# Kernel tuning notes

Hardware: AMD Instinct MI355X
Metric: run time of the kernel (lower is better)

## Reference

```python
import jax, jax.numpy as jnp
import numpy as np

N, E, D, L = 100000, 1600000, 32, 5


def setup_inputs() -> dict:
    key = jax.random.key(0)
    ks = jax.random.split(key, 8)
    s = 1.0 / np.sqrt(D)
    return {
        "x": jax.random.normal(ks[0], (N, D), dtype=jnp.float32),
        "edge_attr": jax.random.normal(ks[1], (E, D), dtype=jnp.float32),
        "edge_index": jax.random.randint(ks[2], (2, E), 0, N, dtype=jnp.int64),
        "W1": jax.random.normal(ks[3], (L, D, D), dtype=jnp.float32) * s,
        "b1": jnp.zeros((L, D), dtype=jnp.float32),
        "W2": jax.random.normal(ks[4], (L, D, D), dtype=jnp.float32) * s,
        "b2": jnp.zeros((L, D), dtype=jnp.float32),
        "eps": jnp.zeros((L,), dtype=jnp.float32),  # train_eps=True, init 0
    }


def reference(x, edge_attr, edge_index, W1, b1, W2, b2, eps):
    # GINEConv x num_layers: aggr_i = sum_j relu(x_j + e_ij); out = MLP((1+eps)*x_i + aggr_i)
    src = edge_index[0]  # j (message source)
    dst = edge_index[1]  # i (message target)
    n = x.shape[0]
    for l in range(W1.shape[0]):
        msg = jax.nn.relu(x[src] + edge_attr)                  # [E, D]
        aggr = jax.ops.segment_sum(msg, dst, num_segments=n)    # [N, D]
        h = (1.0 + eps[l]) * x + aggr
        h = jax.nn.relu(h @ W1[l] + b1[l]) @ W2[l] + b2[l]      # inner MLP
        x = jax.nn.relu(h)                                      # outer relu in forward
    return x
```

## Files before the change

kernel.cpp:

```cpp
#include <hip/hip_runtime.h>

#define D 32
#define NPB 64
#define SRC_BITS 25
#define SRC_MASK ((1 << SRC_BITS) - 1)
#define SCAN_CHUNK 1024
#define PKCAP 2048

typedef unsigned short ushort_t;

__device__ __forceinline__ float relu_f(float v) { return v > 0.f ? v : 0.f; }

__device__ __forceinline__ unsigned bf16_rne(float f) {
    unsigned u = __float_as_uint(f);
    return (u + 0x7FFFu + ((u >> 16) & 1u)) >> 16;
}
__device__ __forceinline__ float bflo(unsigned u) { return __uint_as_float(u << 16); }
__device__ __forceinline__ float bfhi(unsigned u) { return __uint_as_float(u & 0xFFFF0000u); }

__global__ void __launch_bounds__(256) hist_kernel(
    const int* __restrict__ dst, int* __restrict__ deg, int E)
{
    int e = blockIdx.x * 256 + threadIdx.x;
    if (e < E) atomicAdd(&deg[dst[e]], 1);
}

__global__ void __launch_bounds__(256) scan_partial_kernel(
    const int* __restrict__ deg, int* __restrict__ part, int N)
{
    __shared__ int s[256];
    int t = threadIdx.x;
    int base = blockIdx.x * SCAN_CHUNK + t * 4;
    int sum = 0;
    #pragma unroll
    for (int i = 0; i < 4; ++i) { int idx = base + i; if (idx < N) sum += deg[idx]; }
    s[t] = sum;
    __syncthreads();
    for (int off = 128; off > 0; off >>= 1) {
        if (t < off) s[t] += s[t + off];
        __syncthreads();
    }
    if (t == 0) part[blockIdx.x] = s[0];
}

__global__ void scan_part_exclusive_kernel(int* part, int nb)
{
    if (threadIdx.x == 0 && blockIdx.x == 0) {
        int run = 0;
        for (int i = 0; i < nb; ++i) { int v = part[i]; part[i] = run; run += v; }
    }
}

__global__ void __launch_bounds__(256) scan_final_kernel(
    int* __restrict__ rowdeg, const int* __restrict__ part, int N)
{
    __shared__ int s[256];
    int t = threadIdx.x;
    int base = blockIdx.x * SCAN_CHUNK + t * 4;
    int d0 = 0, d1 = 0, d2 = 0, d3 = 0;
    if (base + 0 < N) d0 = rowdeg[base + 0];
    if (base + 1 < N) d1 = rowdeg[base + 1];
    if (base + 2 < N) d2 = rowdeg[base + 2];
    if (base + 3 < N) d3 = rowdeg[base + 3];
    int tsum = d0 + d1 + d2 + d3;
    s[t] = tsum;
    __syncthreads();
    for (int off = 1; off < 256; off <<= 1) {
        int a = (t >= off) ? s[t - off] : 0;
        __syncthreads();
        s[t] += a;
        __syncthreads();
    }
    int excl = s[t] - tsum + part[blockIdx.x];
    if (base + 0 < N) rowdeg[base + 0] = excl;
    if (base + 1 < N) rowdeg[base + 1] = excl + d0;
    if (base + 2 < N) rowdeg[base + 2] = excl + d0 + d1;
    if (base + 3 < N) rowdeg[base + 3] = excl + d0 + d1 + d2;
}

__global__ void __launch_bounds__(256) place_full_kernel(
    const int* __restrict__ src, const int* __restrict__ dst,
    const float* __restrict__ ea, int* __restrict__ row,
    int* __restrict__ srcpk, unsigned* __restrict__ eah, int E)
{
    int i = blockIdx.x * 256 + threadIdx.x;
    if (i >= E * 8) return;
    int e = i >> 3, q = i & 7;
    int pos = 0;
    if (q == 0) {
        int d = dst[e];
        pos = atomicAdd(&row[d], 1);
        srcpk[pos] = src[e] | ((d & (NPB - 1)) << SRC_BITS);
    }
    pos = __shfl(pos, 0, 8);
    float4 v = reinterpret_cast<const float4*>(ea)[(size_t)e * 8 + q];
    uint2 w;
    w.x = bf16_rne(v.x) | (bf16_rne(v.y) << 16);
    w.y = bf16_rne(v.z) | (bf16_rne(v.w) << 16);
    reinterpret_cast<uint2*>(eah)[(size_t)pos * 8 + q] = w;
}

__global__ void __launch_bounds__(256) place_csr_kernel(
    const int* __restrict__ src, const int* __restrict__ dst,
    int* __restrict__ row, int* __restrict__ srcperm,
    int* __restrict__ eperm, int E)
{
    int e = blockIdx.x * 256 + threadIdx.x;
    if (e < E) {
        int pos = atomicAdd(&row[dst[e]], 1);
        srcperm[pos] = src[e] | ((dst[e] & (NPB - 1)) << SRC_BITS);
        eperm[pos] = e;
    }
}

__global__ void __launch_bounds__(256) x2h_kernel(
    const float* __restrict__ x, ushort_t* __restrict__ xh, int n)
{
    int i = blockIdx.x * 256 + threadIdx.x;
    if (i < n) xh[i] = (ushort_t)bf16_rne(x[i]);
}

template <bool LAST>
__global__ void __launch_bounds__(256, 4) gine_fused7_kernel(
    const uint2* __restrict__ xh2,
    const uint2* __restrict__ eah,
    const int* __restrict__ srcpk, const int* __restrict__ row,
    const float* __restrict__ W1, const float* __restrict__ b1,
    const float* __restrict__ W2, const float* __restrict__ b2,
    const float* __restrict__ eps, int l,
    ushort_t* __restrict__ outh, float* __restrict__ outf, int N)
{
    __shared__ float aggr[NPB][D];
    __shared__ float W1s[D * D], W2s[D * D];
    __shared__ float b1s[D], b2s[D];
    __shared__ float ys[8][D];
    __shared__ int   pkL[PKCAP];

    int t = threadIdx.x;
    int n0 = blockIdx.x * NPB;
    int nlast = min(n0 + NPB - 1, N - 1);
    int estart = n0 ? row[n0 - 1] : 0;
    int eend   = row[nlast];
    int EB = eend - estart;
    int staged = min(EB, PKCAP);

    for (int i = t; i < D * D; i += 256) { W1s[i] = W1[i]; W2s[i] = W2[i]; }
    if (t < D) { b1s[t] = b1[t]; b2s[t] = b2[t]; }
    for (int i = t; i < NPB * D; i += 256) ((float*)aggr)[i] = 0.f;
    for (int i = t; i < staged; i += 256) pkL[i] = srcpk[estart + i];
    __syncthreads();

    int g8 = t >> 3;
    int q  = t & 7;

    int chunk = (staged + 31) >> 5;
    int a = min(g8 * chunk, staged);
    int b = min(a + chunk, staged);

    float4 acc = make_float4(0.f, 0.f, 0.f, 0.f);
    int cur = -1;

    auto flush = [&]() {
        if (cur >= 0) {
            atomicAdd(&aggr[cur][q * 4 + 0], acc.x);
            atomicAdd(&aggr[cur][q * 4 + 1], acc.y);
            atomicAdd(&aggr[cur][q * 4 + 2], acc.z);
            atomicAdd(&aggr[cur][q * 4 + 3], acc.w);
        }
    };
    auto edge = [&](int ld, uint2 ew, uint2 xw) {
        if (ld != cur) {
            flush();
            cur = ld;
            acc = make_float4(0.f, 0.f, 0.f, 0.f);
        }
        acc.x += relu_f(bflo(xw.x) + bflo(ew.x));
        acc.y += relu_f(bfhi(xw.x) + bfhi(ew.x));
        acc.z += relu_f(bflo(xw.y) + bflo(ew.y));
        acc.w += relu_f(bfhi(xw.y) + bfhi(ew.y));
    };

    uint2 wA[4], wB[4], xA[4], xB[4];
    int   pA[4], pB[4];

    auto loadA = [&](int base) {
        #pragma unroll
        for (int i = 0; i < 4; ++i) {
            int p = pkL[base + i];
            pA[i] = p;
            wA[i] = eah[(size_t)(estart + base + i) * 8 + q];
            xA[i] = xh2[(size_t)(p & SRC_MASK) * 8 + q];
        }
    };
    auto loadB = [&](int base) {
        #pragma unroll
        for (int i = 0; i < 4; ++i) {
            int p = pkL[base + i];
            pB[i] = p;
            wB[i] = eah[(size_t)(estart + base + i) * 8 + q];
            xB[i] = xh2[(size_t)(p & SRC_MASK) * 8 + q];
        }
    };
    auto computeA = [&]() {
        #pragma unroll
        for (int i = 0; i < 4; ++i)
            edge((pA[i] >> SRC_BITS) & (NPB - 1), wA[i], xA[i]);
    };
    auto computeB = [&]() {
        #pragma unroll
        for (int i = 0; i < 4; ++i)
            edge((pB[i] >> SRC_BITS) & (NPB - 1), wB[i], xB[i]);
    };

    int nfull = (b - a) >> 2;
    int k = a;
    if (nfull > 0) loadA(k);
    int i = 0;
    for (; i + 2 <= nfull; i += 2) {
        loadB(k + 4);
        computeA();
        if (i + 2 < nfull) loadA(k + 8);
        computeB();
        k += 8;
    }
    if (i < nfull) { computeA(); k += 4; }

    for (int e = k; e < b; ++e) {
        int p = pkL[e];
        uint2 w = eah[(size_t)(estart + e) * 8 + q];
        uint2 xw = xh2[(size_t)(p & SRC_MASK) * 8 + q];
        edge((p >> SRC_BITS) & (NPB - 1), w, xw);
    }
    if (EB > staged) {
        int ovn = EB - staged;
        int c2 = (ovn + 31) >> 5;
        int o0 = staged + min(g8 * c2, ovn);
        int o1 = min(o0 + c2, EB);
        for (int e = o0; e < o1; ++e) {
            int p = srcpk[estart + e];
            uint2 w = eah[(size_t)(estart + e) * 8 + q];
            uint2 xw = xh2[(size_t)(p & SRC_MASK) * 8 + q];
            edge((p >> SRC_BITS) & (NPB - 1), w, xw);
        }
    }
    flush();
    __syncthreads();

    const ushort_t* xhu = (const ushort_t*)xh2;
    int hw = t >> 5, j = t & 31;
    float ep1 = 1.0f + eps[l];
    for (int r = 0; r < 8; ++r) {
        int ln = hw * 8 + r;
        int n = n0 + ln;
        if (n >= N) break;
        float xf = bflo((unsigned)xhu[(size_t)n * D + j]);
        float h = ep1 * xf + aggr[ln][j];
        aggr[ln][j] = h;
        float a1 = b1s[j];
        #pragma unroll
        for (int kk = 0; kk < D; ++kk)
            a1 = fmaf(aggr[ln][kk], W1s[kk * D + j], a1);
        float y = relu_f(a1);
        ys[hw][j] = y;
        float a2 = b2s[j];
        #pragma unroll
        for (int kk = 0; kk < D; ++kk)
            a2 = fmaf(ys[hw][kk], W2s[kk * D + j], a2);
        float o = relu_f(a2);
        if (LAST) outf[(size_t)n * D + j] = o;
        else      outh[(size_t)n * D + j] = (ushort_t)bf16_rne(o);
    }
}

__global__ void __launch_bounds__(256) gine_fused_kernel(
    const float* __restrict__ x, const float* __restrict__ ea,
    const int* __restrict__ srcperm, const int* __restrict__ eperm,
    const int* __restrict__ row,
    const float* __restrict__ W1, const float* __restrict__ b1,
    const float* __restrict__ W2, const float* __restrict__ b2,
    const float* __restrict__ eps, int l, float* __restrict__ out, int N)
{
    __shared__ float W1s[D * D], W2s[D * D], b1s[D], b2s[D];
    int t = threadIdx.x;
    for (int i = t; i < D * D; i += 256) { W1s[i] = W1[i]; W2s[i] = W2[i]; }
    if (t < D) { b1s[t] = b1[t]; b2s[t] = b2[t]; }
    __syncthreads();

    int g = t >> 5, j = t & 31;
    int node = blockIdx.x * 8 + g;
    if (node >= N) return;
    int start = node ? row[node - 1] : 0;
    int end = row[node];

    float acc = 0.f;
    for (int k = start; k < end; ++k) {
        int s0 = srcperm[k] & SRC_MASK;
        float e0 = ea[(size_t)eperm[k] * D + j];
        acc += relu_f(x[(size_t)s0 * D + j] + e0);
    }
    float h = (1.0f + eps[l]) * x[(size_t)node * D + j] + acc;
    float a1 = b1s[j];
    #pragma unroll
    for (int kk = 0; kk < D; ++kk)
        a1 = fmaf(__shfl(h, kk, 32), W1s[kk * D + j], a1);
    float y = relu_f(a1);
    float a2 = b2s[j];
    #pragma unroll
    for (int kk = 0; kk < D; ++kk)
        a2 = fmaf(__shfl(y, kk, 32), W2s[kk * D + j], a2);
    out[(size_t)node * D + j] = relu_f(a2);
}

__global__ void __launch_bounds__(256) gine_scatter_kernel(
    const float* __restrict__ x, const float* __restrict__ ea,
    const int* __restrict__ src, const int* __restrict__ dst,
    float* __restrict__ aggr, int E)
{
    int i = blockIdx.x * blockDim.x + threadIdx.x;
    if (i >= E * 8) return;
    int e = i >> 3, q = i & 7;
    float4 a = reinterpret_cast<const float4*>(ea)[(size_t)e * 8 + q];
    int s = src[e], d = dst[e];
    float4 xv = reinterpret_cast<const float4*>(x)[(size_t)s * 8 + q];
    float* base = aggr + (size_t)d * D + (size_t)q * 4;
    __hip_atomic_fetch_add(base + 0, relu_f(xv.x + a.x), __ATOMIC_RELAXED, __HIP_MEMORY_SCOPE_AGENT);
    __hip_atomic_fetch_add(base + 1, relu_f(xv.y + a.y), __ATOMIC_RELAXED, __HIP_MEMORY_SCOPE_AGENT);
    __hip_atomic_fetch_add(base + 2, relu_f(xv.z + a.z), __ATOMIC_RELAXED, __HIP_MEMORY_SCOPE_AGENT);
    __hip_atomic_fetch_add(base + 3, relu_f(xv.w + a.w), __ATOMIC_RELAXED, __HIP_MEMORY_SCOPE_AGENT);
}

__global__ void __launch_bounds__(256) gine_node_kernel(
    const float* __restrict__ x, const float* __restrict__ aggr,
    const float* __restrict__ W1, const float* __restrict__ b1,
    const float* __restrict__ W2, const float* __restrict__ b2,
    const float* __restrict__ eps, int l, float* __restrict__ out, int N)
{
    __shared__ float W1s[D * D], W2s[D * D], b1s[D], b2s[D];
    __shared__ float hs[8][D], y1s[8][D];
    int t = threadIdx.x;
    for (int i = t; i < D * D; i += 256) { W1s[i] = W1[i]; W2s[i] = W2[i]; }
    if (t < D) { b1s[t] = b1[t]; b2s[t] = b2[t]; }
    float ep1 = 1.0f + eps[l];
    int local = t >> 5, j = t & 31;
    int node = blockIdx.x * 8 + local;
    __syncthreads();
    if (node < N)
        hs[local][j] = ep1 * x[(size_t)node * D + j] + aggr[(size_t)node * D + j];
    __syncthreads();
    if (node < N) {
        float acc = b1s[j];
        #pragma unroll
        for (int k = 0; k < D; ++k) acc = fmaf(hs[local][k], W1s[k * D + j], acc);
        y1s[local][j] = relu_f(acc);
    }
    __syncthreads();
    if (node < N) {
        float acc = b2s[j];
        #pragma unroll
        for (int k = 0; k < D; ++k) acc = fmaf(y1s[local][k], W2s[k * D + j], acc);
        out[(size_t)node * D + j] = relu_f(acc);
    }
}

extern "C" void kernel_launch(void* const* d_in, const int* in_sizes, int n_in,
                              void* d_out, int out_size, void* d_ws, size_t ws_size,
                              hipStream_t stream) {
    const float* x_in = (const float*)d_in[0];
    const float* ea   = (const float*)d_in[1];
    const int*   ei   = (const int*)d_in[2];
    const float* W1   = (const float*)d_in[3];
    const float* b1   = (const float*)d_in[4];
    const float* W2   = (const float*)d_in[5];
    const float* b2   = (const float*)d_in[6];
    const float* eps  = (const float*)d_in[7];

    int N = in_sizes[0] / D;
    int E = in_sizes[1] / D;
    int L = in_sizes[3] / (D * D);

    const int* src = ei;
    const int* dst = ei + E;

    float* out = (float*)d_out;
    char*  ws  = (char*)d_ws;

    size_t off = 0;
    auto take = [&](size_t bytes) -> size_t {
        size_t p = off; off = (off + bytes + 255) & ~(size_t)255; return p;
    };
    size_t o_bufA    = take((size_t)N * D * sizeof(float));
    size_t o_row     = take((size_t)(N + 8) * sizeof(int));
    size_t o_part    = take(1024 * sizeof(int));
    size_t o_srcpk   = take((size_t)E * sizeof(int));
    size_t o_eperm   = take((size_t)E * sizeof(int));
    size_t need_csr  = off;
    size_t o_eah     = take((size_t)E * D * sizeof(ushort_t));
    size_t need_full = off;
    size_t o_xhA     = take((size_t)N * D * sizeof(ushort_t));
    size_t o_xhB     = take((size_t)N * D * sizeof(ushort_t));
    size_t need_xh   = off;

    float* bufA  = (float*)(ws + o_bufA);
    int*   row   = (int*)(ws + o_row);
    int*   part  = (int*)(ws + o_part);
    int*   srcpk = (int*)(ws + o_srcpk);
    int*   eperm = (int*)(ws + o_eperm);

    int path = (ws_size >= need_xh) ? 3
             : (ws_size >= need_full) ? 2
             : (ws_size >= need_csr) ? 1 : 0;

    if (path == 0) {
        float* aggr = bufA + (size_t)N * D;
        const float* cur = x_in;
        for (int l = 0; l < L; ++l) {
            float* nxt = (((L - 1 - l) & 1) == 0) ? out : bufA;
            hipMemsetAsync(aggr, 0, (size_t)N * D * sizeof(float), stream);
            gine_scatter_kernel<<<(E * 8 + 255) / 256, 256, 0, stream>>>(cur, ea, src, dst, aggr, E);
            gine_node_kernel<<<(N + 7) / 8, 256, 0, stream>>>(
                cur, aggr, W1 + (size_t)l * D * D, b1 + (size_t)l * D,
                W2 + (size_t)l * D * D, b2 + (size_t)l * D, eps, l, nxt, N);
            cur = nxt;
        }
        return;
    }

    unsigned* eah = (unsigned*)(ws + o_eah);

    int nb = (N + SCAN_CHUNK - 1) / SCAN_CHUNK;
    hipMemsetAsync(row, 0, (size_t)N * sizeof(int), stream);
    hist_kernel<<<(E + 255) / 256, 256, 0, stream>>>(dst, row, E);
    scan_partial_kernel<<<nb, 256, 0, stream>>>(row, part, N);
    scan_part_exclusive_kernel<<<1, 64, 0, stream>>>(part, nb);
    scan_final_kernel<<<nb, 256, 0, stream>>>(row, part, N);
    if (path >= 2) {
        place_full_kernel<<<(E * 8 + 255) / 256, 256, 0, stream>>>(
            src, dst, ea, row, srcpk, eah, E);
    } else {
        place_csr_kernel<<<(E + 255) / 256, 256, 0, stream>>>(
            src, dst, row, srcpk, eperm, E);
    }

    if (path == 3) {
        ushort_t* xhA = (ushort_t*)(ws + o_xhA);
        ushort_t* xhB = (ushort_t*)(ws + o_xhB);
        x2h_kernel<<<(N * D + 255) / 256, 256, 0, stream>>>(x_in, xhA, N * D);

        ushort_t* curh = xhA;
        ushort_t* nxth = xhB;
        int nblk = (N + NPB - 1) / NPB;
        for (int l = 0; l < L; ++l) {
            bool last = (l == L - 1);
            if (last) {
                gine_fused7_kernel<true><<<nblk, 256, 0, stream>>>(
                    (const uint2*)curh, (const uint2*)eah, srcpk, row,
                    W1 + (size_t)l * D * D, b1 + (size_t)l * D,
                    W2 + (size_t)l * D * D, b2 + (size_t)l * D, eps, l,
                    nullptr, out, N);
            } else {
                gine_fused7_kernel<false><<<nblk, 256, 0, stream>>>(
                    (const uint2*)curh, (const uint2*)eah, srcpk, row,
                    W1 + (size_t)l * D * D, b1 + (size_t)l * D,
                    W2 + (size_t)l * D * D, b2 + (size_t)l * D, eps, l,
                    nxth, nullptr, N);
                ushort_t* tmp = curh; curh = nxth; nxth = tmp;
            }
        }
        return;
    }

    const float* cur = x_in;
    for (int l = 0; l < L; ++l) {
        float* nxt = (((L - 1 - l) & 1) == 0) ? out : bufA;
        gine_fused_kernel<<<(N + 7) / 8, 256, 0, stream>>>(
            cur, ea, srcpk, eperm, row,
            W1 + (size_t)l * D * D, b1 + (size_t)l * D,
            W2 + (size_t)l * D * D, b2 + (size_t)l * D, eps, l, nxt, N);
        cur = nxt;
    }
}
```

Baseline: 515.2 us.

## Interleave edge-attribute pairs for 16-byte loads and use nontemporal placement

Stores the bf16 edge attributes so that each pair of consecutive CSR edges sits interleaved per 8-byte lane slot. The aggregation loop can then fetch two edges per uint4 load instead of one per uint2, with a peel step to keep the pair aligned. The placement kernel also switches to nontemporal loads and stores for the streamed edge data. This cuts the number of load instructions in the gather loop, at the cost of extra peel logic and a slightly padded buffer. The workspace path selection is also simplified.

```diff
diff --git a/kernel.cpp b/kernel.cpp
--- a/kernel.cpp
+++ b/kernel.cpp
@@ -17,6 +17,10 @@
 }
 __device__ __forceinline__ float bflo(unsigned u) { return __uint_as_float(u << 16); }
 __device__ __forceinline__ float bfhi(unsigned u) { return __uint_as_float(u & 0xFFFF0000u); }
+
+__device__ __forceinline__ size_t eah_u2(int pos, int q) {
+    return (size_t)((unsigned)pos >> 1) * 16 + q * 2 + (pos & 1);
+}
 
 __global__ void __launch_bounds__(256) hist_kernel(
     const int* __restrict__ dst, int* __restrict__ deg, int E)
@@ -81,7 +85,7 @@
 __global__ void __launch_bounds__(256) place_full_kernel(
     const int* __restrict__ src, const int* __restrict__ dst,
     const float* __restrict__ ea, int* __restrict__ row,
-    int* __restrict__ srcpk, unsigned* __restrict__ eah, int E)
+    int* __restrict__ srcpk, uint2* __restrict__ eah, int E)
 {
     int i = blockIdx.x * 256 + threadIdx.x;
     if (i >= E * 8) return;
@@ -90,14 +94,19 @@
     if (q == 0) {
         int d = dst[e];
         pos = atomicAdd(&row[d], 1);
-        srcpk[pos] = src[e] | ((d & (NPB - 1)) << SRC_BITS);
+        __builtin_nontemporal_store(src[e] | ((d & (NPB - 1)) << SRC_BITS), &srcpk[pos]);
     }
     pos = __shfl(pos, 0, 8);
-    float4 v = reinterpret_cast<const float4*>(ea)[(size_t)e * 8 + q];
-    uint2 w;
-    w.x = bf16_rne(v.x) | (bf16_rne(v.y) << 16);
-    w.y = bf16_rne(v.z) | (bf16_rne(v.w) << 16);
-    reinterpret_cast<uint2*>(eah)[(size_t)pos * 8 + q] = w;
+    const float* eap = ea + ((size_t)e * 8 + q) * 4;
+    float vx = __builtin_nontemporal_load(eap + 0);
+    float vy = __builtin_nontemporal_load(eap + 1);
+    float vz = __builtin_nontemporal_load(eap + 2);
+    float vw = __builtin_nontemporal_load(eap + 3);
+    unsigned long long w =
+        (unsigned long long)(bf16_rne(vx) | (bf16_rne(vy) << 16)) |
+        ((unsigned long long)(bf16_rne(vz) | (bf16_rne(vw) << 16)) << 32);
+    __builtin_nontemporal_store(
+        w, reinterpret_cast<unsigned long long*>(eah + eah_u2(pos, q)));
 }
 
 __global__ void __launch_bounds__(256) place_csr_kernel(
@@ -121,7 +130,7 @@
 }
 
 template <bool LAST>
-__global__ void __launch_bounds__(256, 4) gine_fused7_kernel(
+__global__ void __launch_bounds__(256, 4) gine_fused8_kernel(
     const uint2* __restrict__ xh2,
     const uint2* __restrict__ eah,
     const int* __restrict__ srcpk, const int* __restrict__ row,
@@ -136,6 +145,8 @@
     __shared__ float ys[8][D];
     __shared__ int   pkL[PKCAP];
 
+    const uint4* eah4 = reinterpret_cast<const uint4*>(eah);
+
     int t = threadIdx.x;
     int n0 = blockIdx.x * NPB;
     int nlast = min(n0 + NPB - 1, N - 1);
@@ -179,41 +190,57 @@
         acc.z += relu_f(bflo(xw.y) + bflo(ew.y));
         acc.w += relu_f(bfhi(xw.y) + bfhi(ew.y));
     };
-
-    uint2 wA[4], wB[4], xA[4], xB[4];
+    auto single = [&](int e, int pk) {
+        uint2 w = eah[eah_u2(estart + e, q)];
+        uint2 xw = xh2[(size_t)(pk & SRC_MASK) * 8 + q];
+        edge((pk >> SRC_BITS) & (NPB - 1), w, xw);
+    };
+
+    uint4 eA[2], eB[2];
+    uint2 xA[4], xB[4];
     int   pA[4], pB[4];
 
     auto loadA = [&](int base) {
+        int gp = estart + base;
+        eA[0] = eah4[((size_t)((unsigned)gp >> 1)) * 8 + q];
+        eA[1] = eah4[((size_t)((unsigned)(gp + 2) >> 1)) * 8 + q];
         #pragma unroll
         for (int i = 0; i < 4; ++i) {
             int p = pkL[base + i];
             pA[i] = p;
-            wA[i] = eah[(size_t)(estart + base + i) * 8 + q];
             xA[i] = xh2[(size_t)(p & SRC_MASK) * 8 + q];
         }
     };
     auto loadB = [&](int base) {
+        int gp = estart + base;
+        eB[0] = eah4[((size_t)((unsigned)gp >> 1)) * 8 + q];
+        eB[1] = eah4[((size_t)((unsigned)(gp + 2) >> 1)) * 8 + q];
         #pragma unroll
         for (int i = 0; i < 4; ++i) {
             int p = pkL[base + i];
             pB[i] = p;
-            wB[i] = eah[(size_t)(estart + base + i) * 8 + q];
             xB[i] = xh2[(size_t)(p & SRC_MASK) * 8 + q];
         }
     };
     auto computeA = [&]() {
-        #pragma unroll
-        for (int i = 0; i < 4; ++i)
-            edge((pA[i] >> SRC_BITS) & (NPB - 1), wA[i], xA[i]);
+        edge((pA[0] >> SRC_BITS) & (NPB - 1), make_uint2(eA[0].x, eA[0].y), xA[0]);
+        edge((pA[1] >> SRC_BITS) & (NPB - 1), make_uint2(eA[0].z, eA[0].w), xA[1]);
+        edge((pA[2] >> SRC_BITS) & (NPB - 1), make_uint2(eA[1].x, eA[1].y), xA[2]);
+        edge((pA[3] >> SRC_BITS) & (NPB - 1), make_uint2(eA[1].z, eA[1].w), xA[3]);
     };
     auto computeB = [&]() {
-        #pragma unroll
-        for (int i = 0; i < 4; ++i)
-            edge((pB[i] >> SRC_BITS) & (NPB - 1), wB[i], xB[i]);
-    };
-
-    int nfull = (b - a) >> 2;
+        edge((pB[0] >> SRC_BITS) & (NPB - 1), make_uint2(eB[0].x, eB[0].y), xB[0]);
+        edge((pB[1] >> SRC_BITS) & (NPB - 1), make_uint2(eB[0].z, eB[0].w), xB[1]);
+        edge((pB[2] >> SRC_BITS) & (NPB - 1), make_uint2(eB[1].x, eB[1].y), xB[2]);
+        edge((pB[3] >> SRC_BITS) & (NPB - 1), make_uint2(eB[1].z, eB[1].w), xB[3]);
+    };
+
     int k = a;
+    if (k < b && ((estart + k) & 1)) {
+        single(k, pkL[k]);
+        ++k;
+    }
+    int nfull = (b - k) >> 2;
     if (nfull > 0) loadA(k);
     int i = 0;
     for (; i + 2 <= nfull; i += 2) {
@@ -225,23 +252,14 @@
     }
     if (i < nfull) { computeA(); k += 4; }
 
-    for (int e = k; e < b; ++e) {
-        int p = pkL[e];
-        uint2 w = eah[(size_t)(estart + e) * 8 + q];
-        uint2 xw = xh2[(size_t)(p & SRC_MASK) * 8 + q];
-        edge((p >> SRC_BITS) & (NPB - 1), w, xw);
-    }
+    for (int e = k; e < b; ++e) single(e, pkL[e]);
+
     if (EB > staged) {
         int ovn = EB - staged;
         int c2 = (ovn + 31) >> 5;
         int o0 = staged + min(g8 * c2, ovn);
         int o1 = min(o0 + c2, EB);
-        for (int e = o0; e < o1; ++e) {
-            int p = srcpk[estart + e];
-            uint2 w = eah[(size_t)(estart + e) * 8 + q];
-            uint2 xw = xh2[(size_t)(p & SRC_MASK) * 8 + q];
-            edge((p >> SRC_BITS) & (NPB - 1), w, xw);
-        }
+        for (int e = o0; e < o1; ++e) single(e, srcpk[estart + e]);
     }
     flush();
     __syncthreads();
@@ -394,11 +412,10 @@
     size_t o_srcpk   = take((size_t)E * sizeof(int));
     size_t o_eperm   = take((size_t)E * sizeof(int));
     size_t need_csr  = off;
-    size_t o_eah     = take((size_t)E * D * sizeof(ushort_t));
-    size_t need_full = off;
+    size_t o_eah     = take((((size_t)E + 1) / 2) * 128);
     size_t o_xhA     = take((size_t)N * D * sizeof(ushort_t));
     size_t o_xhB     = take((size_t)N * D * sizeof(ushort_t));
-    size_t need_xh   = off;
+    size_t need_full = off;
 
     float* bufA  = (float*)(ws + o_bufA);
     int*   row   = (int*)(ws + o_row);
@@ -406,9 +423,7 @@
     int*   srcpk = (int*)(ws + o_srcpk);
     int*   eperm = (int*)(ws + o_eperm);
 
-    int path = (ws_size >= need_xh) ? 3
-             : (ws_size >= need_full) ? 2
-             : (ws_size >= need_csr) ? 1 : 0;
+    int path = (ws_size >= need_full) ? 3 : (ws_size >= need_csr ? 1 : 0);
 
     if (path == 0) {
         float* aggr = bufA + (size_t)N * D;
@@ -425,41 +440,35 @@
         return;
     }
 
-    unsigned* eah = (unsigned*)(ws + o_eah);
-
     int nb = (N + SCAN_CHUNK - 1) / SCAN_CHUNK;
     hipMemsetAsync(row, 0, (size_t)N * sizeof(int), stream);
     hist_kernel<<<(E + 255) / 256, 256, 0, stream>>>(dst, row, E);
     scan_partial_kernel<<<nb, 256, 0, stream>>>(row, part, N);
     scan_part_exclusive_kernel<<<1, 64, 0, stream>>>(part, nb);
     scan_final_kernel<<<nb, 256, 0, stream>>>(row, part, N);
-    if (path >= 2) {
+
+    if (path == 3) {
+        uint2*    eah = (uint2*)(ws + o_eah);
+        ushort_t* xhA = (ushort_t*)(ws + o_xhA);
+        ushort_t* xhB = (ushort_t*)(ws + o_xhB);
+
         place_full_kernel<<<(E * 8 + 255) / 256, 256, 0, stream>>>(
             src, dst, ea, row, srcpk, eah, E);
-    } else {
-        place_csr_kernel<<<(E + 255) / 256, 256, 0, stream>>>(
-            src, dst, row, srcpk, eperm, E);
-    }
-
-    if (path == 3) {
-        ushort_t* xhA = (ushort_t*)(ws + o_xhA);
-        ushort_t* xhB = (ushort_t*)(ws + o_xhB);
         x2h_kernel<<<(N * D + 255) / 256, 256, 0, stream>>>(x_in, xhA, N * D);
 
         ushort_t* curh = xhA;
         ushort_t* nxth = xhB;
         int nblk = (N + NPB - 1) / NPB;
         for (int l = 0; l < L; ++l) {
-            bool last = (l == L - 1);
-            if (last) {
-                gine_fused7_kernel<true><<<nblk, 256, 0, stream>>>(
-                    (const uint2*)curh, (const uint2*)eah, srcpk, row,
+            if (l == L - 1) {
+                gine_fused8_kernel<true><<<nblk, 256, 0, stream>>>(
+                    (const uint2*)curh, eah, srcpk, row,
                     W1 + (size_t)l * D * D, b1 + (size_t)l * D,
                     W2 + (size_t)l * D * D, b2 + (size_t)l * D, eps, l,
                     nullptr, out, N);
             } else {
-                gine_fused7_kernel<false><<<nblk, 256, 0, stream>>>(
-                    (const uint2*)curh, (const uint2*)eah, srcpk, row,
+                gine_fused8_kernel<false><<<nblk, 256, 0, stream>>>(
+                    (const uint2*)curh, eah, srcpk, row,
                     W1 + (size_t)l * D * D, b1 + (size_t)l * D,
                     W2 + (size_t)l * D * D, b2 + (size_t)l * D, eps, l,
                     nxth, nullptr, N);
@@ -469,6 +478,8 @@
         return;
     }
 
+    place_csr_kernel<<<(E + 255) / 256, 256, 0, stream>>>(
+        src, dst, row, srcpk, eperm, E);
     const float* cur = x_in;
     for (int l = 0; l < L; ++l) {
         float* nxt = (((L - 1 - l) & 1) == 0) ? out : bufA;
```

Measured after the change: 575.4 us. +11.7%, slower.
